# Optimization experiments

Measured on AMD Instinct MI355X. Metric: run time of the kernel, lower is better.

Reference implementation:

```python
import jax, jax.numpy as jnp
import numpy as np

K = 1.0  # Lorentz curvature
N, H, IN_S, OUT_S = 4096, 12, 256, 128  # nodes, heads, spatial in/out dims


def _midpoint_norm(ave):
    # Lorentz midpoint normalization: sqrt(K) * ave / sqrt(|<ave,ave>_L|)
    inner = -ave[..., 0:1] ** 2 + jnp.sum(ave[..., 1:] ** 2, axis=-1, keepdims=True)
    denom = jnp.sqrt(jnp.maximum(jnp.abs(inner), 1e-8))
    return jnp.sqrt(K) * ave / denom


def setup_inputs() -> dict:
    key = jax.random.key(0)
    ks = jax.random.split(key, 8)
    xs = jax.random.normal(ks[0], (N, IN_S), jnp.float32)
    xt = jnp.sqrt(jnp.sum(xs * xs, axis=-1, keepdims=True) + K)
    x_lorentz = jnp.concatenate([xt, xs], axis=-1)  # [N, 257] on the manifold
    std = 1.0 / np.sqrt(IN_S)
    def lin(k1, k2):
        W = jax.random.uniform(k1, (H, OUT_S, IN_S), jnp.float32, -std, std)
        b = jax.random.uniform(k2, (H, OUT_S), jnp.float32, -std, std)
        return W, b
    Wq, bq = lin(ks[1], ks[2])
    Wk, bk = lin(ks[3], ks[4])
    Wv, bv = lin(ks[5], ks[6])
    scale = jnp.array([np.sqrt(OUT_S + 1)], jnp.float32)  # sqrt(out_channels)
    bias = jnp.zeros((), jnp.float32)
    return {"x_lorentz": x_lorentz, "Wq": Wq, "bq": bq, "Wk": Wk, "bk": bk,
            "Wv": Wv, "bv": bv, "scale": scale, "bias": bias}


def reference(x_lorentz, Wq, bq, Wk, bk, Wv, bv, scale, bias):
    xs = x_lorentz[..., 1:]  # drop time coord: [N, IN_S]

    def hyp_linear(W, b):
        # per-head linear on spatial part, then reconstruct Lorentz time coord
        s = jnp.einsum('ni,hoi->hno', xs, W) + b[:, None, :]  # [H, N, OUT_S]
        t = jnp.sqrt(jnp.sum(s * s, axis=-1, keepdims=True) + K)
        return jnp.concatenate([t, s], axis=-1)  # [H, N, OUT_S+1]

    q = hyp_linear(Wq, bq)
    k = hyp_linear(Wk, bk)
    v = hyp_linear(Wv, bv)

    # Lorentz inner product scores: <q,k>_L = -q0*k0 + q_s . k_s
    sgn = jnp.concatenate([-jnp.ones((1,), q.dtype), jnp.ones((q.shape[-1] - 1,), q.dtype)])
    att = 2.0 + 2.0 * jnp.einsum('hnd,hmd->hnm', q * sgn, k)  # [H, N, N]
    att = att / scale + bias
    att = jax.nn.softmax(att, axis=-1)

    # weighted Lorentz midpoint per head
    ave = jnp.einsum('hnm,hmd->hnd', att, v)
    out = _midpoint_norm(ave)           # [H, N, D]
    out = out.transpose(1, 0, 2)        # [N, H, D]
    # uniform midpoint across heads
    out = _midpoint_norm(out.mean(axis=-2))  # [N, D]
    return out
```

## Files before the change

### kernel.cpp

```cpp
#include <hip/hip_runtime.h>
#include <hip/hip_bf16.h>

#define NT   4096
#define NH   12
#define INS  256
#define DOUT 128
#define D1   129
#define PSTR 132

typedef __attribute__((ext_vector_type(8))) short bf16x8;
typedef __attribute__((ext_vector_type(4))) float f32x4;

__device__ __forceinline__ short f2bf(float f) {
  union { __hip_bfloat16 h; short s; } u;
  u.h = __float2bfloat16(f);
  return u.s;
}
__device__ __forceinline__ float bf2f(short s) {
  union { unsigned u; float f; } v;
  v.u = ((unsigned)(unsigned short)s) << 16;
  return v.f;
}

#define MFMA16(a,b,c) __builtin_amdgcn_mfma_f32_16x16x32_bf16((a),(b),(c),0,0,0)

#define GL2LDS(gp, lp) \
  __builtin_amdgcn_global_load_lds((const __attribute__((address_space(1))) unsigned*)(gp), \
                                   (__attribute__((address_space(3))) unsigned*)(lp), 16, 0, 0)


__global__ void k_cvt_xs(const float* __restrict__ xl, short* __restrict__ xs) {
  int i = blockIdx.x * 256 + threadIdx.x;
  int row = i >> 8, col = i & 255;
  xs[i] = f2bf(xl[row * 257 + 1 + col]);
}

__global__ void k_cvt_w(const float* __restrict__ w0, const float* __restrict__ w1,
                        const float* __restrict__ w2, short* __restrict__ dst) {
  int i = blockIdx.x * 256 + threadIdx.x;
  const float* s = blockIdx.y == 0 ? w0 : (blockIdx.y == 1 ? w1 : w2);
  dst[(size_t)blockIdx.y * (NH * DOUT * INS) + i] = f2bf(s[i]);
}


__launch_bounds__(256, 2)
__global__ void k_proj(const short* __restrict__ xs, const short* __restrict__ Wb,
                       const float* __restrict__ b0, const float* __restrict__ b1,
                       const float* __restrict__ b2,
                       short* __restrict__ Qb, short* __restrict__ Kb, short* __restrict__ VT,
                       float* __restrict__ qt, float* __restrict__ kt, float* __restrict__ vt) {
  __shared__ __align__(16) short vlds[128][144];
  int t = threadIdx.x, l = t & 63, w = t >> 6;
  int lr = l & 15, lg = l >> 4;
  int h = blockIdx.y, z = blockIdx.z;
  int n0w = blockIdx.x * 128 + w * 32;
  const short* Wh = Wb + ((size_t)z * NH + h) * DOUT * INS;
  const float* bias = z == 0 ? b0 : (z == 1 ? b1 : b2);

  f32x4 acc[2][8] = {};
#pragma unroll
  for (int dk = 0; dk < 8; ++dk) {
    bf16x8 a[2], b[8];
#pragma unroll
    for (int qf = 0; qf < 2; ++qf)
      a[qf] = *(const bf16x8*)(xs + (size_t)(n0w + 16 * qf + lr) * INS + dk * 32 + lg * 8);
#pragma unroll
    for (int cf = 0; cf < 8; ++cf)
      b[cf] = *(const bf16x8*)(Wh + (size_t)(lr + 16 * cf) * INS + dk * 32 + lg * 8);
#pragma unroll
    for (int qf = 0; qf < 2; ++qf)
#pragma unroll
      for (int cf = 0; cf < 8; ++cf)
        acc[qf][cf] = MFMA16(a[qf], b[cf], acc[qf][cf]);
  }

  float tval[2][4];
#pragma unroll
  for (int qf = 0; qf < 2; ++qf) {
    float ssq[4] = {0.f, 0.f, 0.f, 0.f};
#pragma unroll
    for (int cf = 0; cf < 8; ++cf) {
      float bv = bias[h * DOUT + lr + 16 * cf];
#pragma unroll
      for (int r = 0; r < 4; ++r) {
        acc[qf][cf][r] += bv;
        ssq[r] += acc[qf][cf][r] * acc[qf][cf][r];
      }
    }
#pragma unroll
    for (int r = 0; r < 4; ++r) {
      float s = ssq[r];
      s += __shfl_xor(s, 1); s += __shfl_xor(s, 2);
      s += __shfl_xor(s, 4); s += __shfl_xor(s, 8);
      tval[qf][r] = sqrtf(s + 1.0f);
    }
  }

  if (z < 2) {
    short* Ob = (z == 0) ? Qb : Kb;
    float* Ot = (z == 0) ? qt : kt;
#pragma unroll
    for (int qf = 0; qf < 2; ++qf)
#pragma unroll
      for (int r = 0; r < 4; ++r) {
        int n = n0w + 16 * qf + lg * 4 + r;
#pragma unroll
        for (int cf = 0; cf < 8; ++cf)
          Ob[((size_t)h * NT + n) * DOUT + lr + 16 * cf] = f2bf(acc[qf][cf][r]);
        if (lr == 0) Ot[(size_t)h * NT + n] = tval[qf][r];
      }
  } else {
#pragma unroll
    for (int qf = 0; qf < 2; ++qf)
#pragma unroll
      for (int cf = 0; cf < 8; ++cf)
#pragma unroll
        for (int r = 0; r < 4; ++r) {
          int nl = w * 32 + 16 * qf + lg * 4 + r;
          vlds[lr + 16 * cf][nl] = f2bf(acc[qf][cf][r]);
        }
#pragma unroll
    for (int qf = 0; qf < 2; ++qf)
#pragma unroll
      for (int r = 0; r < 4; ++r) {
        int n = n0w + 16 * qf + lg * 4 + r;
        if (lr == 0) vt[(size_t)h * NT + n] = tval[qf][r];
      }
    __syncthreads();
    int d = t >> 1, half = t & 1;
    const short* src = &vlds[d][half * 64];
    short* dst = VT + ((size_t)h * DOUT + d) * NT + blockIdx.x * 128 + half * 64;
#pragma unroll
    for (int j = 0; j < 8; ++j)
      *(bf16x8*)(dst + j * 8) = *(const bf16x8*)(src + j * 8);
  }
}


#define PROWB 144
#define PWAVE (32 * PROWB)

__launch_bounds__(256, 2)
__global__ void k_attn(const short* __restrict__ Qb, const short* __restrict__ Kb,
                       const short* __restrict__ VT,
                       const float* __restrict__ qt, const float* __restrict__ ktp,
                       const float* __restrict__ vtp,
                       const float* __restrict__ scalep, float* __restrict__ part) {
  __shared__ __align__(16) char lds_k[64 * 256];
  __shared__ __align__(16) char lds_v[128 * 128];
  __shared__ __align__(16) char lds_p[4 * PWAVE];

  int t = threadIdx.x, l = t & 63, w = t >> 6;
  int lr = l & 15, lg = l >> 4;
  int h = blockIdx.y, z = blockIdx.z;
  int n0w = blockIdx.x * 128 + w * 32;
  float c1 = 2.0f / scalep[0];

  const short* Qh = Qb + (size_t)h * NT * DOUT;
  const short* Kh = Kb + (size_t)h * NT * DOUT;
  const short* VTh = VT + (size_t)h * DOUT * NT;
  const float* qth = qt + (size_t)h * NT;
  const float* kth = ktp + (size_t)h * NT;
  const float* vth = vtp + (size_t)h * NT;

  bf16x8 aq[2][4];
#pragma unroll
  for (int qf = 0; qf < 2; ++qf)
#pragma unroll
    for (int dk = 0; dk < 4; ++dk)
      aq[qf][dk] = *(const bf16x8*)(Qh + (size_t)(n0w + 16 * qf + lr) * DOUT + dk * 32 + lg * 8);
  float qc[2][4];
#pragma unroll
  for (int qf = 0; qf < 2; ++qf)
#pragma unroll
    for (int r = 0; r < 4; ++r)
      qc[qf][r] = c1 * qth[n0w + 16 * qf + lg * 4 + r];

  f32x4 accO[2][8] = {};
  float l_run[2][4] = {}, avt_run[2][4] = {};

  for (int ktile = 0; ktile < NT / 128; ++ktile) {
    int m0 = z * (NT / 2) + ktile * 64;
    __syncthreads();
#pragma unroll
    for (int it = 0; it < 4; ++it) {
      int c = t + it * 256;
      int m = c >> 4, s = c & 15;
      GL2LDS(Kh + (size_t)(m0 + m) * DOUT + ((s ^ (m & 7)) * 8), lds_k + c * 16);
    }
#pragma unroll
    for (int it = 0; it < 4; ++it) {
      int c = t + it * 256;
      int d = c >> 3, s = c & 7;
      GL2LDS(VTh + (size_t)d * NT + m0 + ((s ^ (d & 7)) * 8), lds_v + c * 16);
    }
    float ktv[4], vtv[4];
#pragma unroll
    for (int mf = 0; mf < 4; ++mf) {
      ktv[mf] = kth[m0 + lr + 16 * mf];
      vtv[mf] = vth[m0 + lr + 16 * mf];
    }
    __syncthreads();

    f32x4 accS[2][4] = {};
#pragma unroll
    for (int dk = 0; dk < 4; ++dk) {
      bf16x8 bk[4];
#pragma unroll
      for (int mf = 0; mf < 4; ++mf) {
        int m = lr + 16 * mf;
        int slot = (4 * dk + lg) ^ (m & 7);
        bk[mf] = *(const bf16x8*)(lds_k + m * 256 + slot * 16);
      }
#pragma unroll
      for (int qf = 0; qf < 2; ++qf)
#pragma unroll
        for (int mf = 0; mf < 4; ++mf)
          accS[qf][mf] = MFMA16(aq[qf][dk], bk[mf], accS[qf][mf]);
    }

#pragma unroll
    for (int qf = 0; qf < 2; ++qf) {
#pragma unroll
      for (int r = 0; r < 4; ++r) {
        int ql = lg * 4 + r + 16 * qf;
        short* prow = (short*)(lds_p + w * PWAVE + ql * PROWB);
        float ps = 0.f, pv = 0.f;
#pragma unroll
        for (int mf = 0; mf < 4; ++mf) {
          float a = fmaf(-qc[qf][r], ktv[mf], c1 * accS[qf][mf][r]);
          float p = __expf(a);
          short pb = f2bf(p);
          prow[lr + 16 * mf] = pb;
          float pr = bf2f(pb);
          ps += pr;
          pv += pr * vtv[mf];
        }
        l_run[qf][r]   += ps;
        avt_run[qf][r] += pv;
      }
    }

#pragma unroll
    for (int ks = 0; ks < 2; ++ks) {
      bf16x8 ap[2];
#pragma unroll
      for (int qf = 0; qf < 2; ++qf)
        ap[qf] = *(const bf16x8*)(lds_p + w * PWAVE + (16 * qf + lr) * PROWB + ks * 64 + lg * 16);
      bf16x8 bv[8];
#pragma unroll
      for (int df = 0; df < 8; ++df) {
        int d = lr + 16 * df;
        int slot = (4 * ks + lg) ^ (d & 7);
        bv[df] = *(const bf16x8*)(lds_v + d * 128 + slot * 16);
      }
#pragma unroll
      for (int qf = 0; qf < 2; ++qf)
#pragma unroll
        for (int df = 0; df < 8; ++df)
          accO[qf][df] = MFMA16(ap[qf], bv[df], accO[qf][df]);
    }
  }

#pragma unroll
  for (int qf = 0; qf < 2; ++qf)
#pragma unroll
    for (int r = 0; r < 4; ++r) {
      float lv = l_run[qf][r];
      lv += __shfl_xor(lv, 1); lv += __shfl_xor(lv, 2);
      lv += __shfl_xor(lv, 4); lv += __shfl_xor(lv, 8);
      float av = avt_run[qf][r];
      av += __shfl_xor(av, 1); av += __shfl_xor(av, 2);
      av += __shfl_xor(av, 4); av += __shfl_xor(av, 8);
      int n = n0w + 16 * qf + lg * 4 + r;
      float* base = part + ((size_t)h * NT + n) * PSTR;
#pragma unroll
      for (int df = 0; df < 8; ++df)
        atomicAdd(base + lr + 16 * df, accO[qf][df][r]);
      if (lr == 0) { atomicAdd(base + 128, av); atomicAdd(base + 129, lv); }
    }
}


__global__ void k_comb(const float* __restrict__ part, float* __restrict__ out) {
  int l = threadIdx.x & 63, w = threadIdx.x >> 6;
  int n = blockIdx.x * 4 + w;
  float acc_lo = 0.f, acc_hi = 0.f, acc_t = 0.f;
#pragma unroll
  for (int h = 0; h < NH; ++h) {
    const float* p = part + ((size_t)h * NT + n) * PSTR;
    float x = p[l], y = p[64 + l], pvt = p[128], pl = p[129];
    float inv = 1.0f / pl;
    float olo = x * inv, ohi = y * inv, at = pvt * inv;
    float sp = olo * olo + ohi * ohi;
    sp += __shfl_xor(sp, 1);  sp += __shfl_xor(sp, 2);
    sp += __shfl_xor(sp, 4);  sp += __shfl_xor(sp, 8);
    sp += __shfl_xor(sp, 16); sp += __shfl_xor(sp, 32);
    float inner = sp - at * at;
    float rd = 1.0f / sqrtf(fmaxf(fabsf(inner), 1e-8f));
    acc_lo += olo * rd; acc_hi += ohi * rd; acc_t += at * rd;
  }
  const float m = 1.0f / (float)NH;
  float vlo = acc_lo * m, vhi = acc_hi * m, vt = acc_t * m;
  float sp = vlo * vlo + vhi * vhi;
  sp += __shfl_xor(sp, 1);  sp += __shfl_xor(sp, 2);
  sp += __shfl_xor(sp, 4);  sp += __shfl_xor(sp, 8);
  sp += __shfl_xor(sp, 16); sp += __shfl_xor(sp, 32);
  float inner = sp - vt * vt;
  float rd = 1.0f / sqrtf(fmaxf(fabsf(inner), 1e-8f));
  float* orow = out + (size_t)n * D1;
  orow[1 + l] = vlo * rd;
  orow[65 + l] = vhi * rd;
  if (l == 0) orow[0] = vt * rd;
}


extern "C" void kernel_launch(void* const* d_in, const int* in_sizes, int n_in,
                              void* d_out, int out_size, void* d_ws, size_t ws_size,
                              hipStream_t stream) {
  (void)in_sizes; (void)n_in; (void)out_size; (void)ws_size;
  const float* xl    = (const float*)d_in[0];
  const float* Wq    = (const float*)d_in[1];
  const float* bq    = (const float*)d_in[2];
  const float* Wk    = (const float*)d_in[3];
  const float* bk    = (const float*)d_in[4];
  const float* Wv    = (const float*)d_in[5];
  const float* bv    = (const float*)d_in[6];
  const float* scale = (const float*)d_in[7];
  float* out = (float*)d_out;

  char* ws = (char*)d_ws;
  size_t off = 0;
  auto alloc = [&](size_t b) { char* p = ws + off; off = (off + b + 255) & ~(size_t)255; return p; };
  short* xs    = (short*)alloc((size_t)NT * INS * 2);
  short* Wb    = (short*)alloc((size_t)3 * NH * DOUT * INS * 2);
  short* Qb    = (short*)alloc((size_t)NH * NT * DOUT * 2);
  short* Kb    = (short*)alloc((size_t)NH * NT * DOUT * 2);
  short* VT    = (short*)alloc((size_t)NH * DOUT * NT * 2);
  float* qt    = (float*)alloc((size_t)NH * NT * 4);
  float* kt    = (float*)alloc((size_t)NH * NT * 4);
  float* vt    = (float*)alloc((size_t)NH * NT * 4);
  float* part  = (float*)alloc((size_t)NH * NT * PSTR * 4);

  hipMemsetAsync(part, 0, (size_t)NH * NT * PSTR * 4, stream);
  k_cvt_xs<<<NT, 256, 0, stream>>>(xl, xs);
  k_cvt_w<<<dim3(NH * DOUT * INS / 256, 3), 256, 0, stream>>>(Wq, Wk, Wv, Wb);
  k_proj<<<dim3(NT / 128, NH, 3), 256, 0, stream>>>(xs, Wb, bq, bk, bv, Qb, Kb, VT, qt, kt, vt);
  k_attn<<<dim3(NT / 128, NH, 2), 256, 0, stream>>>(Qb, Kb, VT, qt, kt, vt, scale, part);
  k_comb<<<NT / 4, 256, 0, stream>>>(part, out);
}
```

Before: 343.4 us.

## Prefetch next K tile, fold score scale into Q, drop softmax row sums

```diff
diff --git a/kernel.cpp b/kernel.cpp
--- a/kernel.cpp
+++ b/kernel.cpp
@@ -46,7 +46,7 @@
 __launch_bounds__(256, 2)
 __global__ void k_proj(const short* __restrict__ xs, const short* __restrict__ Wb,
                        const float* __restrict__ b0, const float* __restrict__ b1,
-                       const float* __restrict__ b2,
+                       const float* __restrict__ b2, const float* __restrict__ scalep,
                        short* __restrict__ Qb, short* __restrict__ Kb, short* __restrict__ VT,
                        float* __restrict__ qt, float* __restrict__ kt, float* __restrict__ vt) {
   __shared__ __align__(16) short vlds[128][144];
@@ -97,6 +97,7 @@
   }
 
   if (z < 2) {
+    float f = (z == 0) ? (2.0f * 1.442695040888963f / scalep[0]) : 1.0f;
     short* Ob = (z == 0) ? Qb : Kb;
     float* Ot = (z == 0) ? qt : kt;
 #pragma unroll
@@ -106,8 +107,8 @@
         int n = n0w + 16 * qf + lg * 4 + r;
 #pragma unroll
         for (int cf = 0; cf < 8; ++cf)
-          Ob[((size_t)h * NT + n) * DOUT + lr + 16 * cf] = f2bf(acc[qf][cf][r]);
-        if (lr == 0) Ot[(size_t)h * NT + n] = tval[qf][r];
+          Ob[((size_t)h * NT + n) * DOUT + lr + 16 * cf] = f2bf(acc[qf][cf][r] * f);
+        if (lr == 0) Ot[(size_t)h * NT + n] = tval[qf][r] * f;
       }
   } else {
 #pragma unroll
@@ -144,8 +145,7 @@
 __global__ void k_attn(const short* __restrict__ Qb, const short* __restrict__ Kb,
                        const short* __restrict__ VT,
                        const float* __restrict__ qt, const float* __restrict__ ktp,
-                       const float* __restrict__ vtp,
-                       const float* __restrict__ scalep, float* __restrict__ part) {
+                       const float* __restrict__ vtp, float* __restrict__ part) {
   __shared__ __align__(16) char lds_k[64 * 256];
   __shared__ __align__(16) char lds_v[128 * 128];
   __shared__ __align__(16) char lds_p[4 * PWAVE];
@@ -154,7 +154,6 @@
   int lr = l & 15, lg = l >> 4;
   int h = blockIdx.y, z = blockIdx.z;
   int n0w = blockIdx.x * 128 + w * 32;
-  float c1 = 2.0f / scalep[0];
 
   const short* Qh = Qb + (size_t)h * NT * DOUT;
   const short* Kh = Kb + (size_t)h * NT * DOUT;
@@ -169,25 +168,33 @@
 #pragma unroll
     for (int dk = 0; dk < 4; ++dk)
       aq[qf][dk] = *(const bf16x8*)(Qh + (size_t)(n0w + 16 * qf + lr) * DOUT + dk * 32 + lg * 8);
-  float qc[2][4];
+  float qc2[2][4];
 #pragma unroll
   for (int qf = 0; qf < 2; ++qf)
 #pragma unroll
     for (int r = 0; r < 4; ++r)
-      qc[qf][r] = c1 * qth[n0w + 16 * qf + lg * 4 + r];
+      qc2[qf][r] = qth[n0w + 16 * qf + lg * 4 + r];
 
   f32x4 accO[2][8] = {};
-  float l_run[2][4] = {}, avt_run[2][4] = {};
-
-  for (int ktile = 0; ktile < NT / 128; ++ktile) {
-    int m0 = z * (NT / 2) + ktile * 64;
-    __syncthreads();
+  float avt_run[2][4] = {};
+
+  int kc_m = t >> 2, kc_s = (t & 3);
+  (void)kc_m; (void)kc_s;
+
+  {
+    int m0 = z * (NT / 2);
 #pragma unroll
     for (int it = 0; it < 4; ++it) {
       int c = t + it * 256;
       int m = c >> 4, s = c & 15;
       GL2LDS(Kh + (size_t)(m0 + m) * DOUT + ((s ^ (m & 7)) * 8), lds_k + c * 16);
     }
+  }
+
+  for (int ktile = 0; ktile < NT / 128; ++ktile) {
+    int m0 = z * (NT / 2) + ktile * 64;
+    __syncthreads();
+
 #pragma unroll
     for (int it = 0; it < 4; ++it) {
       int c = t + it * 256;
@@ -200,7 +207,6 @@
       ktv[mf] = kth[m0 + lr + 16 * mf];
       vtv[mf] = vth[m0 + lr + 16 * mf];
     }
-    __syncthreads();
 
     f32x4 accS[2][4] = {};
 #pragma unroll
@@ -225,19 +231,29 @@
       for (int r = 0; r < 4; ++r) {
         int ql = lg * 4 + r + 16 * qf;
         short* prow = (short*)(lds_p + w * PWAVE + ql * PROWB);
-        float ps = 0.f, pv = 0.f;
+        float pv = 0.f;
 #pragma unroll
         for (int mf = 0; mf < 4; ++mf) {
-          float a = fmaf(-qc[qf][r], ktv[mf], c1 * accS[qf][mf][r]);
-          float p = __expf(a);
+          float a2 = fmaf(-qc2[qf][r], ktv[mf], accS[qf][mf][r]);
+          float p;
+          asm("v_exp_f32 %0, %1" : "=v"(p) : "v"(a2));
           short pb = f2bf(p);
           prow[lr + 16 * mf] = pb;
-          float pr = bf2f(pb);
-          ps += pr;
-          pv += pr * vtv[mf];
+          pv = fmaf(bf2f(pb), vtv[mf], pv);
         }
-        l_run[qf][r]   += ps;
         avt_run[qf][r] += pv;
+      }
+    }
+
+    __syncthreads();
+
+    if (ktile + 1 < NT / 128) {
+      int m1 = m0 + 64;
+#pragma unroll
+      for (int it = 0; it < 4; ++it) {
+        int c = t + it * 256;
+        int m = c >> 4, s = c & 15;
+        GL2LDS(Kh + (size_t)(m1 + m) * DOUT + ((s ^ (m & 7)) * 8), lds_k + c * 16);
       }
     }
 
@@ -266,9 +282,6 @@
   for (int qf = 0; qf < 2; ++qf)
 #pragma unroll
     for (int r = 0; r < 4; ++r) {
-      float lv = l_run[qf][r];
-      lv += __shfl_xor(lv, 1); lv += __shfl_xor(lv, 2);
-      lv += __shfl_xor(lv, 4); lv += __shfl_xor(lv, 8);
       float av = avt_run[qf][r];
       av += __shfl_xor(av, 1); av += __shfl_xor(av, 2);
       av += __shfl_xor(av, 4); av += __shfl_xor(av, 8);
@@ -277,7 +290,7 @@
 #pragma unroll
       for (int df = 0; df < 8; ++df)
         atomicAdd(base + lr + 16 * df, accO[qf][df][r]);
-      if (lr == 0) { atomicAdd(base + 128, av); atomicAdd(base + 129, lv); }
+      if (lr == 0) atomicAdd(base + 128, av);
     }
 }
 
@@ -289,29 +302,25 @@
 #pragma unroll
   for (int h = 0; h < NH; ++h) {
     const float* p = part + ((size_t)h * NT + n) * PSTR;
-    float x = p[l], y = p[64 + l], pvt = p[128], pl = p[129];
-    float inv = 1.0f / pl;
-    float olo = x * inv, ohi = y * inv, at = pvt * inv;
-    float sp = olo * olo + ohi * ohi;
+    float x = p[l], y = p[64 + l], at = p[128];
+    float sp = x * x + y * y;
     sp += __shfl_xor(sp, 1);  sp += __shfl_xor(sp, 2);
     sp += __shfl_xor(sp, 4);  sp += __shfl_xor(sp, 8);
     sp += __shfl_xor(sp, 16); sp += __shfl_xor(sp, 32);
     float inner = sp - at * at;
     float rd = 1.0f / sqrtf(fmaxf(fabsf(inner), 1e-8f));
-    acc_lo += olo * rd; acc_hi += ohi * rd; acc_t += at * rd;
-  }
-  const float m = 1.0f / (float)NH;
-  float vlo = acc_lo * m, vhi = acc_hi * m, vt = acc_t * m;
-  float sp = vlo * vlo + vhi * vhi;
+    acc_lo += x * rd; acc_hi += y * rd; acc_t += at * rd;
+  }
+  float sp = acc_lo * acc_lo + acc_hi * acc_hi;
   sp += __shfl_xor(sp, 1);  sp += __shfl_xor(sp, 2);
   sp += __shfl_xor(sp, 4);  sp += __shfl_xor(sp, 8);
   sp += __shfl_xor(sp, 16); sp += __shfl_xor(sp, 32);
-  float inner = sp - vt * vt;
+  float inner = sp - acc_t * acc_t;
   float rd = 1.0f / sqrtf(fmaxf(fabsf(inner), 1e-8f));
   float* orow = out + (size_t)n * D1;
-  orow[1 + l] = vlo * rd;
-  orow[65 + l] = vhi * rd;
-  if (l == 0) orow[0] = vt * rd;
+  orow[1 + l] = acc_lo * rd;
+  orow[65 + l] = acc_hi * rd;
+  if (l == 0) orow[0] = acc_t * rd;
 }
 
 
@@ -345,7 +354,7 @@
   hipMemsetAsync(part, 0, (size_t)NH * NT * PSTR * 4, stream);
   k_cvt_xs<<<NT, 256, 0, stream>>>(xl, xs);
   k_cvt_w<<<dim3(NH * DOUT * INS / 256, 3), 256, 0, stream>>>(Wq, Wk, Wv, Wb);
-  k_proj<<<dim3(NT / 128, NH, 3), 256, 0, stream>>>(xs, Wb, bq, bk, bv, Qb, Kb, VT, qt, kt, vt);
-  k_attn<<<dim3(NT / 128, NH, 2), 256, 0, stream>>>(Qb, Kb, VT, qt, kt, vt, scale, part);
+  k_proj<<<dim3(NT / 128, NH, 3), 256, 0, stream>>>(xs, Wb, bq, bk, bv, scale, Qb, Kb, VT, qt, kt, vt);
+  k_attn<<<dim3(NT / 128, NH, 2), 256, 0, stream>>>(Qb, Kb, VT, qt, kt, vt, part);
   k_comb<<<NT / 4, 256, 0, stream>>>(part, out);
 }
```

New measurement: 323.2 us. 1.06x faster.
